# Kernel optimization log

Hardware: AMD Instinct MI355X
Metric: run time of the kernel (lower is better)

Reference implementation:

```python
import jax, jax.numpy as jnp
import numpy as np

B, R, N, D = 8, 5, 1024, 512  # batch, relations, utterances per dialogue, d_model
LN_EPS = 1e-5


def setup_inputs() -> dict:
    key = jax.random.key(0)
    k1, k2, k3 = jax.random.split(key, 3)
    h = jax.random.normal(k1, (B, N, D), dtype=jnp.float32)
    # Binary adjacency: adj[b, r, v, u] = 1 means u sends a message to v under relation r.
    adj = (jax.random.uniform(k2, (B, R, N, N)) < 0.5).astype(jnp.float32)
    # Relation 0 is the self-loop relation (identity), as in build_adjacency.
    adj = adj.at[:, 0].set(jnp.broadcast_to(jnp.eye(N, dtype=jnp.float32), (B, N, N)))
    # Per-relation Linear (bias=False) weights, torch convention: y = x @ W_r.T, W_r: (D, D)
    W = jax.random.normal(k3, (R, D, D), dtype=jnp.float32) * 0.02
    gamma = jnp.ones((D,), dtype=jnp.float32)
    beta = jnp.zeros((D,), dtype=jnp.float32)
    return {"h": h, "adj": adj, "W": W, "gamma": gamma, "beta": beta}


def reference(h, adj, W, gamma, beta):
    # Degree-normalize each relation's adjacency (row-normalized mean aggregation).
    deg = jnp.clip(jnp.sum(adj, axis=-1, keepdims=True), 1.0)  # (B,R,N,1)
    A = adj / deg
    # Mean aggregation per relation: (B,R,N,N) @ (B,N,D) -> (B,R,N,D)
    msg = jnp.einsum('brvu,bud->brvd', A, h)
    # Per-relation linear (x @ W_r.T) and sum over relations: (B,N,D)
    agg = jnp.einsum('brvd,red->bve', msg, W)
    # Dropout is identity in eval mode; ReLU, residual, LayerNorm.
    out = jax.nn.relu(agg) + h
    mu = jnp.mean(out, axis=-1, keepdims=True)
    xc = out - mu
    var = jnp.mean(xc * xc, axis=-1, keepdims=True)
    return xc / jnp.sqrt(var + LN_EPS) * gamma + beta
```

## Files before the change

kernel.cpp:

```cpp
#include <hip/hip_runtime.h>
#include <stdint.h>

#define Bd 8
#define Rr 5
#define Nn 1024
#define Dd 512
#define KK (Rr*Dd)

typedef __attribute__((ext_vector_type(8))) short bf16x8;
typedef __attribute__((ext_vector_type(4))) float f32x4;
typedef unsigned short u16;

__device__ __forceinline__ u16 f2bf(float x){
  union { float f; unsigned u; } v; v.f = x;
  unsigned r = v.u + 0x7FFFu + ((v.u >> 16) & 1u);
  return (u16)(r >> 16);
}

__device__ __forceinline__ void gll16(const void* g, void* l){
  __builtin_amdgcn_global_load_lds(
      (const __attribute__((address_space(1))) void*)g,
      (__attribute__((address_space(3))) void*)l, 16, 0, 0);
}

__global__ __launch_bounds__(256) void k_prep(
    const float* __restrict__ h, const float* __restrict__ W,
    u16* __restrict__ hTp, u16* __restrict__ Wt2, u16* __restrict__ msg){
  __shared__ float t32[32][65];
  const int tid = threadIdx.x;
  const int g = blockIdx.x;
  if (g < 2048){
    const int ut  = g & 31;
    const int dtg = (g >> 5) & 7;
    const int b   = g >> 8;
    const float* hb = h + ((size_t)b*Nn + (size_t)ut*32)*Dd + dtg*64;
    #pragma unroll
    for (int j=0;j<8;j++){
      int e = j*256 + tid;
      int ul = e >> 6, dl = e & 63;
      t32[ul][dl] = hb[(size_t)ul*Dd + dl];
    }
    __syncthreads();
    u16* ob = hTp + (size_t)b*Dd*Nn;
    #pragma unroll
    for (int j=0;j<8;j++){
      int e = j*256 + tid;
      int dtl = e >> 9;
      int rem = e & 511;
      int dr = rem >> 5, uu = rem & 31;
      int dt = dtg*4 + dtl;
      ob[((size_t)ut*32 + dt)*512 + rem] = f2bf(t32[uu][dtl*16 + dr]);
    }
  } else if (g < 3328){
    int idx = (g - 2048)*1024 + tid*4;
    int e = idx / KK;
    int k = idx % KK;
    int ri = (k < 2048) ? (1 + (k >> 9)) : 0;
    int d = k & 511;
    f32x4 w = *(const f32x4*)(W + (((size_t)ri*Dd + e)*Dd + d));
    u16 o[4] = { f2bf(w.x), f2bf(w.y), f2bf(w.z), f2bf(w.w) };
    *(uint2*)(Wt2 + idx) = *(uint2*)o;
  } else {
    int q = g - 3328;
    int row = q*4 + (tid >> 6);
    int d0 = (tid & 63)*8;
    f32x4 a = *(const f32x4*)(h + (size_t)row*Dd + d0);
    f32x4 c = *(const f32x4*)(h + (size_t)row*Dd + d0 + 4);
    bf16x8 pk;
    pk[0]=(short)f2bf(a.x); pk[1]=(short)f2bf(a.y);
    pk[2]=(short)f2bf(a.z); pk[3]=(short)f2bf(a.w);
    pk[4]=(short)f2bf(c.x); pk[5]=(short)f2bf(c.y);
    pk[6]=(short)f2bf(c.z); pk[7]=(short)f2bf(c.w);
    *(bf16x8*)(msg + (size_t)row*KK + 2048 + d0) = pk;
  }
}

__global__ __launch_bounds__(512,2) void k_msg(
    const float* __restrict__ adj, const u16* __restrict__ hTp,
    u16* __restrict__ msg){
  __shared__ __align__(16) u16 sA[2][4][32*64];
  __shared__ float sT[16*516];
  __shared__ float sDeg[4][32];

  const int tid  = threadIdx.x;
  const int lane = tid & 63;
  const int wave = tid >> 6;
  const int b  = blockIdx.x & 7;
  const int vt = blockIdx.x >> 3;
  const int v0 = vt * 32;
  const float* adjb = adj + (((size_t)b*Rr + 1)*Nn + v0)*Nn;
  const u16* hTpb = hTp + (size_t)b*Dd*Nn;

  const int srow = tid >> 4;
  const int sc   = tid & 15;
  const size_t aoff = (size_t)srow*Nn + sc*4;
  const int wslot = sc ^ ((srow & 7) << 1);

  float deg[4] = {0.f,0.f,0.f,0.f};
  f32x4 aregA[4], aregB[4];
  f32x4 acc[4][2][4];
  #pragma unroll
  for (int ri=0;ri<4;ri++)
    #pragma unroll
    for (int m=0;m<2;m++)
      #pragma unroll
      for (int n=0;n<4;n++) acc[ri][m][n] = (f32x4){0.f,0.f,0.f,0.f};

  const int rlo = lane & 15, ch = lane >> 4;
  const int boff = rlo*32 + ch*8;

  #define AISSUE(DST, T) do {                                                 \
    _Pragma("unroll")                                                         \
    for (int ri=0;ri<4;ri++)                                                  \
      DST[ri] = *(const f32x4*)(adjb + (size_t)ri*Nn*Nn + (size_t)(T)*64 + aoff); \
  } while(0)

  #define PACK(SRC, BUFI) do {                                                \
    _Pragma("unroll")                                                         \
    for (int ri=0;ri<4;ri++){                                                 \
      f32x4 p = SRC[ri];                                                      \
      deg[ri] += p.x+p.y+p.z+p.w;                                             \
      uint2 pk;                           \
      pk.x = (__float_as_uint(p.x)>>16) | (__float_as_uint(p.y) & 0xFFFF0000u);\
      pk.y = (__float_as_uint(p.z)>>16) | (__float_as_uint(p.w) & 0xFFFF0000u);\
      *(uint2*)((char*)sA[BUFI][ri] + srow*128 + wslot*8) = pk;               \
    }                                                                         \
  } while(0)

  #define LOADB(DST, T) do {                                                  \
    _Pragma("unroll")                                                         \
    for (int kk=0;kk<2;kk++){                                                 \
      const u16* bp = hTpb + ((((size_t)((T)*2+kk))*32 + (wave<<2))<<9) + boff;\
      _Pragma("unroll")                                                       \
      for (int n=0;n<4;n++)                                                   \
        DST[kk][n] = *(const bf16x8*)(bp + ((size_t)n<<9));                   \
    }                                                                         \
  } while(0)

  #define MSTEP(BFR, BUFI) do {                                               \
    const char* abase = (const char*)sA[BUFI];                                \
    _Pragma("unroll")                                                         \
    for (int kk=0;kk<2;kk++){                                                 \
      _Pragma("unroll")                                                       \
      for (int ri=0;ri<4;ri++){                                               \
        bf16x8 af[2];                                                         \
        _Pragma("unroll")                                                     \
        for (int m=0;m<2;m++){                                                \
          const int row = m*16 + rlo;                                         \
          af[m] = *(const bf16x8*)(abase + ri*4096 + row*128                  \
                    + (((kk*8 + ch*2) ^ ((row&7)<<1))<<3));                   \
        }                                                                     \
        _Pragma("unroll")                                                     \
        for (int m=0;m<2;m++)                                                 \
          _Pragma("unroll")                                                   \
          for (int n=0;n<4;n++)                                               \
            acc[ri][m][n] = __builtin_amdgcn_mfma_f32_16x16x32_bf16(          \
                af[m], BFR[kk][n], acc[ri][m][n], 0, 0, 0);                   \
      }                                                                       \
    }                                                                         \
  } while(0)

  #define STEP_BARRIER() do {                                                 \
    asm volatile("s_waitcnt lgkmcnt(0)" ::: "memory");                        \
    __builtin_amdgcn_sched_barrier(0);                                        \
    __builtin_amdgcn_s_barrier();                                             \
    __builtin_amdgcn_sched_barrier(0);                                        \
  } while(0)

  AISSUE(aregA, 0);
  PACK(aregA, 0);
  __syncthreads();
  AISSUE(aregA, 1);

  for (int t = 0; t < 14; t += 2){
    {
      bf16x8 bfr[2][4];
      LOADB(bfr, t);
      AISSUE(aregB, t+2);
      PACK(aregA, 1);
      MSTEP(bfr, 0);
      STEP_BARRIER();
    }
    {
      bf16x8 bfr[2][4];
      LOADB(bfr, t+1);
      AISSUE(aregA, t+3);
      PACK(aregB, 0);
      MSTEP(bfr, 1);
      STEP_BARRIER();
    }
  }
  {
    bf16x8 bfr[2][4];
    LOADB(bfr, 14);
    PACK(aregA, 1);
    MSTEP(bfr, 0);
    STEP_BARRIER();
  }
  {
    bf16x8 bfr[2][4];
    LOADB(bfr, 15);
    MSTEP(bfr, 1);
  }
  #undef AISSUE
  #undef PACK
  #undef LOADB
  #undef MSTEP
  #undef STEP_BARRIER

  #pragma unroll
  for (int ri=0;ri<4;ri++){
    float d = deg[ri];
    d += __shfl_xor(d, 1); d += __shfl_xor(d, 2);
    d += __shfl_xor(d, 4); d += __shfl_xor(d, 8);
    if (sc == 0) sDeg[ri][srow] = d;
  }
  __syncthreads();

  u16* mb = msg + ((size_t)b*Nn + v0)*KK;
  #pragma unroll
  for (int ri=0;ri<4;ri++){
    #pragma unroll
    for (int hh=0;hh<2;hh++){
      #pragma unroll
      for (int reg=0;reg<4;reg++){
        const int rl = ch*4 + reg;
        const float inv = 1.0f / fmaxf(sDeg[ri][hh*16 + rl], 1.0f);
        #pragma unroll
        for (int n=0;n<4;n++){
          const int col = (wave<<6) + n*16 + rlo;
          const int colw = col ^ (((col>>5)&7)<<2);
          sT[rl*516 + colw] = acc[ri][hh][n][reg] * inv;
        }
      }
      __syncthreads();
      #pragma unroll
      for (int s=0;s<2;s++){
        const int rl = wave*2 + s;
        const int m5 = lane >> 2;
        const int e  = m5 & 7;
        const int j0 = (2*lane) & 7;
        f32x4 lo = *(const f32x4*)&sT[rl*516 + (m5<<5) + (((j0  ) ^ e)<<2)];
        f32x4 hi = *(const f32x4*)&sT[rl*516 + (m5<<5) + (((j0+1) ^ e)<<2)];
        bf16x8 pk;
        pk[0]=(short)f2bf(lo.x); pk[1]=(short)f2bf(lo.y);
        pk[2]=(short)f2bf(lo.z); pk[3]=(short)f2bf(lo.w);
        pk[4]=(short)f2bf(hi.x); pk[5]=(short)f2bf(hi.y);
        pk[6]=(short)f2bf(hi.z); pk[7]=(short)f2bf(hi.w);
        *(bf16x8*)(mb + (size_t)(hh*16 + rl)*KK + ri*512 + lane*8) = pk;
      }
      __syncthreads();
    }
  }
}

__global__ __launch_bounds__(512,4) void k_agg(
    const u16* __restrict__ msg, const u16* __restrict__ Wt,
    float* __restrict__ agg){
  __shared__ __align__(16) u16 sA[2][64*64];
  __shared__ __align__(16) u16 sB[2][128*64];
  const int tid = threadIdx.x;
  const int lane = tid & 63, wave = tid >> 6;
  const int wm = wave >> 2, wn = wave & 3;
  const int g = blockIdx.x;
  const int et = g >> 7;
  const int bv = g & 127;
  const int b  = bv >> 4;
  const int vt = bv & 15;
  const int v0 = vt*64, e0 = et*128;
  const u16* Ab = msg + ((size_t)b*Nn + v0)*KK;
  const u16* Bb = Wt + (size_t)e0*KK;

  f32x4 acc[2][2];
  #pragma unroll
  for (int m=0;m<2;m++)
    #pragma unroll
    for (int n=0;n<2;n++) acc[m][n] = (f32x4){0.f,0.f,0.f,0.f};

  #define STAGE(buf, kt) do {                                              \
    { int c = tid; int row_ = c>>3, chg = (c&7) ^ (row_&7);                \
      gll16(Ab + (size_t)row_*KK + (kt)*64 + chg*8,                        \
            (char*)sA[buf] + ((size_t)(wave<<6))*16); }                    \
    _Pragma("unroll")                                                      \
    for (int i=0;i<2;i++){                                                 \
      int c = i*512 + tid; int row_ = c>>3, chg = (c&7) ^ (row_&7);        \
      gll16(Bb + (size_t)row_*KK + (kt)*64 + chg*8,                        \
            (char*)sB[buf] + ((size_t)(i*512 + (wave<<6)))*16);            \
    }                                                                      \
  } while(0)

  STAGE(0, 0);
  __syncthreads();

  const int ch = lane >> 4, rlo = lane & 15;

  for (int kt = 0; kt < KK/64; ++kt){
    if (kt < KK/64 - 1) STAGE((kt+1)&1, kt+1);
    const char* a  = (const char*)sA[kt&1];
    const char* bb = (const char*)sB[kt&1];
    #pragma unroll
    for (int kk=0; kk<2; ++kk){
      bf16x8 af[2], bfx[2];
      #pragma unroll
      for (int m=0;m<2;m++){
        const int row = wm*32 + m*16 + rlo;
        af[m] = *(const bf16x8*)(a + row*128 + ((((kk<<2)+ch) ^ (row&7))<<4));
      }
      #pragma unroll
      for (int n=0;n<2;n++){
        const int row = wn*32 + n*16 + rlo;
        bfx[n] = *(const bf16x8*)(bb + row*128 + ((((kk<<2)+ch) ^ (row&7))<<4));
      }
      #pragma unroll
      for (int m=0;m<2;m++)
        #pragma unroll
        for (int n=0;n<2;n++)
          acc[m][n] = __builtin_amdgcn_mfma_f32_16x16x32_bf16(af[m], bfx[n], acc[m][n], 0, 0, 0);
    }
    __syncthreads();
  }
  #undef STAGE

  float* ob = agg + ((size_t)b*Nn + v0)*Dd + e0;
  #pragma unroll
  for (int m=0;m<2;m++)
    #pragma unroll
    for (int reg=0;reg<4;reg++){
      const int row = wm*32 + m*16 + ((lane>>4)<<2) + reg;
      #pragma unroll
      for (int n=0;n<2;n++){
        const int col = wn*32 + n*16 + (lane & 15);
        ob[(size_t)row*Dd + col] = acc[m][n][reg];
      }
    }
}

__global__ __launch_bounds__(256,4) void k_ln(
    const float* __restrict__ agg, const float* __restrict__ h,
    const float* __restrict__ gamma, const float* __restrict__ beta,
    float* __restrict__ out){
  const int row = blockIdx.x*4 + (threadIdx.x >> 6);
  const int lane = threadIdx.x & 63;
  const float* a  = agg + (size_t)row*Dd;
  const float* hh = h   + (size_t)row*Dd;
  float x[8];
  float sum = 0.f, sq = 0.f;
  #pragma unroll
  for (int q=0;q<2;q++){
    f32x4 av = *(const f32x4*)(a  + ((size_t)q*64+lane)*4);
    f32x4 hv = *(const f32x4*)(hh + ((size_t)q*64+lane)*4);
    #pragma unroll
    for (int k=0;k<4;k++){
      float v = fmaxf(av[k], 0.f) + hv[k];
      x[q*4+k] = v; sum += v; sq += v*v;
    }
  }
  #pragma unroll
  for (int off=32; off; off>>=1){
    sum += __shfl_xor(sum, off);
    sq  += __shfl_xor(sq,  off);
  }
  const float mu  = sum * (1.f/(float)Dd);
  const float var = sq * (1.f/(float)Dd) - mu*mu;
  const float rstd = rsqrtf(var + 1e-5f);
  float* o = out + (size_t)row*Dd;
  #pragma unroll
  for (int q=0;q<2;q++){
    f32x4 g  = *(const f32x4*)(gamma + ((size_t)q*64+lane)*4);
    f32x4 be = *(const f32x4*)(beta  + ((size_t)q*64+lane)*4);
    f32x4 ov;
    #pragma unroll
    for (int k=0;k<4;k++)
      ov[k] = (x[q*4+k] - mu) * rstd * g[k] + be[k];
    *(f32x4*)(o + ((size_t)q*64+lane)*4) = ov;
  }
}

extern "C" void kernel_launch(void* const* d_in, const int* in_sizes, int n_in,
                              void* d_out, int out_size, void* d_ws, size_t ws_size,
                              hipStream_t stream){
  const float* h     = (const float*)d_in[0];
  const float* adj   = (const float*)d_in[1];
  const float* W     = (const float*)d_in[2];
  const float* gamma = (const float*)d_in[3];
  const float* beta  = (const float*)d_in[4];
  float* out = (float*)d_out;
  char* ws = (char*)d_ws;

  u16*  hTp = (u16*)(ws);
  u16*  Wt2 = (u16*)(ws + 8388608);
  u16*  msg = (u16*)(ws + 11010048);
  float* agg = (float*)(ws + 52953088);

  k_prep<<<dim3(5376), dim3(256), 0, stream>>>(h, W, hTp, Wt2, msg);
  k_msg <<<dim3(Bd*32), dim3(512), 0, stream>>>(adj, hTp, msg);
  k_agg <<<dim3(Bd*(Nn/64)*(Dd/128)), dim3(512), 0, stream>>>(msg, Wt2, agg);
  k_ln  <<<dim3(Bd*Nn/4), dim3(256), 0, stream>>>(agg, h, gamma, beta, out);
}
```

Measured before the change: 95.23 us.

## Split message kernel across D halves with 256-thread blocks and single-buffered loop

Each k_msg block now handles 32 rows and half of the feature dimension with 256 threads, doubling the grid to 512 blocks. The adjacency staging uses 8-float loads per thread with 16-byte LDS writes, the main loop is rewritten into one software-pipelined loop with priority boost around MFMAs, and the epilogue uses a simpler unswizzled transpose with 4-byte stores. This aims to raise occupancy and parallelism, but it reads every adjacency tile twice (once per D half), relying on cache to absorb the duplicate traffic.

```diff
diff --git a/kernel.cpp b/kernel.cpp
--- a/kernel.cpp
+++ b/kernel.cpp
@@ -10,6 +10,7 @@
 typedef __attribute__((ext_vector_type(8))) short bf16x8;
 typedef __attribute__((ext_vector_type(4))) float f32x4;
 typedef unsigned short u16;
+typedef unsigned int u32;
 
 __device__ __forceinline__ u16 f2bf(float x){
   union { float f; unsigned u; } v; v.f = x;
@@ -75,29 +76,32 @@
   }
 }
 
-__global__ __launch_bounds__(512,2) void k_msg(
+__global__ __launch_bounds__(256,2) void k_msg(
     const float* __restrict__ adj, const u16* __restrict__ hTp,
     u16* __restrict__ msg){
   __shared__ __align__(16) u16 sA[2][4][32*64];
-  __shared__ float sT[16*516];
+  __shared__ float sT[16*260];
   __shared__ float sDeg[4][32];
 
   const int tid  = threadIdx.x;
   const int lane = tid & 63;
   const int wave = tid >> 6;
-  const int b  = blockIdx.x & 7;
-  const int vt = blockIdx.x >> 3;
+  const int bid = blockIdx.x;
+  const int dhalf = bid >> 8;
+  const int bv = bid & 255;
+  const int b  = bv >> 5;
+  const int vt = bv & 31;
   const int v0 = vt * 32;
   const float* adjb = adj + (((size_t)b*Rr + 1)*Nn + v0)*Nn;
   const u16* hTpb = hTp + (size_t)b*Dd*Nn;
 
-  const int srow = tid >> 4;
-  const int sc   = tid & 15;
-  const size_t aoff = (size_t)srow*Nn + sc*4;
-  const int wslot = sc ^ ((srow & 7) << 1);
+  const int srow = tid >> 3;
+  const int sc   = tid & 7;
+  const size_t aoff = (size_t)srow*Nn + sc*8;
+  const int wslot = sc ^ (srow & 7);
 
   float deg[4] = {0.f,0.f,0.f,0.f};
-  f32x4 aregA[4], aregB[4];
+  f32x4 ar0[4], ar1[4];
   f32x4 acc[4][2][4];
   #pragma unroll
   for (int ri=0;ri<4;ri++)
@@ -109,36 +113,44 @@
   const int rlo = lane & 15, ch = lane >> 4;
   const int boff = rlo*32 + ch*8;
 
-  #define AISSUE(DST, T) do {                                                 \
-    _Pragma("unroll")                                                         \
-    for (int ri=0;ri<4;ri++)                                                  \
-      DST[ri] = *(const f32x4*)(adjb + (size_t)ri*Nn*Nn + (size_t)(T)*64 + aoff); \
-  } while(0)
-
-  #define PACK(SRC, BUFI) do {                                                \
+  #define AISSUE(T) do {                                                      \
     _Pragma("unroll")                                                         \
     for (int ri=0;ri<4;ri++){                                                 \
-      f32x4 p = SRC[ri];                                                      \
-      deg[ri] += p.x+p.y+p.z+p.w;                                             \
-      uint2 pk;                           \
-      pk.x = (__float_as_uint(p.x)>>16) | (__float_as_uint(p.y) & 0xFFFF0000u);\
-      pk.y = (__float_as_uint(p.z)>>16) | (__float_as_uint(p.w) & 0xFFFF0000u);\
-      *(uint2*)((char*)sA[BUFI][ri] + srow*128 + wslot*8) = pk;               \
+      const float* ap = adjb + (size_t)ri*Nn*Nn + (size_t)(T)*64 + aoff;      \
+      ar0[ri] = *(const f32x4*)ap;                                            \
+      ar1[ri] = *(const f32x4*)(ap + 4);                                      \
     }                                                                         \
   } while(0)
 
-  #define LOADB(DST, T) do {                                                  \
+  #define PACK(BUFI) do {                                                     \
+    _Pragma("unroll")                                                         \
+    for (int ri=0;ri<4;ri++){                                                 \
+      f32x4 p0 = ar0[ri], p1 = ar1[ri];                                       \
+      deg[ri] += p0.x+p0.y+p0.z+p0.w + p1.x+p1.y+p1.z+p1.w;                   \
+      uint4 pk;                           \
+      pk.x = (__float_as_uint(p0.x)>>16) | (__float_as_uint(p0.y) & 0xFFFF0000u);\
+      pk.y = (__float_as_uint(p0.z)>>16) | (__float_as_uint(p0.w) & 0xFFFF0000u);\
+      pk.z = (__float_as_uint(p1.x)>>16) | (__float_as_uint(p1.y) & 0xFFFF0000u);\
+      pk.w = (__float_as_uint(p1.z)>>16) | (__float_as_uint(p1.w) & 0xFFFF0000u);\
+      *(uint4*)((char*)sA[BUFI][ri] + srow*128 + (wslot<<4)) = pk;            \
+    }                                                                         \
+  } while(0)
+
+  #define LOADB(T) do {                                                       \
     _Pragma("unroll")                                                         \
     for (int kk=0;kk<2;kk++){                                                 \
-      const u16* bp = hTpb + ((((size_t)((T)*2+kk))*32 + (wave<<2))<<9) + boff;\
       _Pragma("unroll")                                                       \
-      for (int n=0;n<4;n++)                                                   \
-        DST[kk][n] = *(const bf16x8*)(bp + ((size_t)n<<9));                   \
+      for (int n=0;n<4;n++){                                                  \
+        const int dt = dhalf*16 + (wave<<2) + n;                              \
+        bfr[kk][n] = *(const bf16x8*)(hTpb +                                  \
+            (((size_t)((T)*2+kk)*32 + dt)<<9) + boff);                        \
+      }                                                                       \
     }                                                                         \
   } while(0)
 
-  #define MSTEP(BFR, BUFI) do {                                               \
+  #define MSTEP(BUFI) do {                                                    \
     const char* abase = (const char*)sA[BUFI];                                \
+    __builtin_amdgcn_s_setprio(1);                                            \
     _Pragma("unroll")                                                         \
     for (int kk=0;kk<2;kk++){                                                 \
       _Pragma("unroll")                                                       \
@@ -147,72 +159,61 @@
         _Pragma("unroll")                                                     \
         for (int m=0;m<2;m++){                                                \
           const int row = m*16 + rlo;                                         \
+          const int g = kk*4 + ch;                                            \
           af[m] = *(const bf16x8*)(abase + ri*4096 + row*128                  \
-                    + (((kk*8 + ch*2) ^ ((row&7)<<1))<<3));                   \
+                    + ((g ^ (row&7))<<4));                                    \
         }                                                                     \
         _Pragma("unroll")                                                     \
         for (int m=0;m<2;m++)                                                 \
           _Pragma("unroll")                                                   \
           for (int n=0;n<4;n++)                                               \
             acc[ri][m][n] = __builtin_amdgcn_mfma_f32_16x16x32_bf16(          \
-                af[m], BFR[kk][n], acc[ri][m][n], 0, 0, 0);                   \
+                af[m], bfr[kk][n], acc[ri][m][n], 0, 0, 0);                   \
       }                                                                       \
     }                                                                         \
-  } while(0)
-
+    __builtin_amdgcn_s_setprio(0);                                            \
+  } while(0)
+
+  #define FENCE() __builtin_amdgcn_sched_barrier(0)
   #define STEP_BARRIER() do {                                                 \
     asm volatile("s_waitcnt lgkmcnt(0)" ::: "memory");                        \
-    __builtin_amdgcn_sched_barrier(0);                                        \
+    FENCE();                                                                  \
     __builtin_amdgcn_s_barrier();                                             \
-    __builtin_amdgcn_sched_barrier(0);                                        \
-  } while(0)
-
-  AISSUE(aregA, 0);
-  PACK(aregA, 0);
+    FENCE();                                                                  \
+  } while(0)
+
+  bf16x8 bfr[2][4];
+
+  AISSUE(0);
+  PACK(0);
   __syncthreads();
-  AISSUE(aregA, 1);
-
-  for (int t = 0; t < 14; t += 2){
-    {
-      bf16x8 bfr[2][4];
-      LOADB(bfr, t);
-      AISSUE(aregB, t+2);
-      PACK(aregA, 1);
-      MSTEP(bfr, 0);
-      STEP_BARRIER();
-    }
-    {
-      bf16x8 bfr[2][4];
-      LOADB(bfr, t+1);
-      AISSUE(aregA, t+3);
-      PACK(aregB, 0);
-      MSTEP(bfr, 1);
-      STEP_BARRIER();
-    }
-  }
-  {
-    bf16x8 bfr[2][4];
-    LOADB(bfr, 14);
-    PACK(aregA, 1);
-    MSTEP(bfr, 0);
+  AISSUE(1);
+  FENCE();
+  LOADB(0);
+  FENCE();
+
+  for (int t = 0; t < 15; ++t){
+    PACK((t+1)&1);
+    FENCE();
+    if (t < 14) AISSUE(t+2);
+    FENCE();
+    MSTEP(t&1);
+    FENCE();
+    LOADB(t+1);
     STEP_BARRIER();
   }
-  {
-    bf16x8 bfr[2][4];
-    LOADB(bfr, 15);
-    MSTEP(bfr, 1);
-  }
+  MSTEP(1);
   #undef AISSUE
   #undef PACK
   #undef LOADB
   #undef MSTEP
+  #undef FENCE
   #undef STEP_BARRIER
 
   #pragma unroll
   for (int ri=0;ri<4;ri++){
     float d = deg[ri];
-    d += __shfl_xor(d, 1); d += __shfl_xor(d, 2);
-    d += __shfl_xor(d, 4); d += __shfl_xor(d, 8);
+    d += __shfl_xor(d, 1); d += __shfl_xor(d, 2); d += __shfl_xor(d, 4);
     if (sc == 0) sDeg[ri][srow] = d;
   }
   __syncthreads();
@@ -229,25 +230,22 @@
         #pragma unroll
         for (int n=0;n<4;n++){
           const int col = (wave<<6) + n*16 + rlo;
-          const int colw = col ^ (((col>>5)&7)<<2);
-          sT[rl*516 + colw] = acc[ri][hh][n][reg] * inv;
+          sT[rl*260 + col] = acc[ri][hh][n][reg] * inv;
         }
       }
       __syncthreads();
-      #pragma unroll
-      for (int s=0;s<2;s++){
-        const int rl = wave*2 + s;
-        const int m5 = lane >> 2;
-        const int e  = m5 & 7;
-        const int j0 = (2*lane) & 7;
-        f32x4 lo = *(const f32x4*)&sT[rl*516 + (m5<<5) + (((j0  ) ^ e)<<2)];
-        f32x4 hi = *(const f32x4*)&sT[rl*516 + (m5<<5) + (((j0+1) ^ e)<<2)];
-        bf16x8 pk;
-        pk[0]=(short)f2bf(lo.x); pk[1]=(short)f2bf(lo.y);
-        pk[2]=(short)f2bf(lo.z); pk[3]=(short)f2bf(lo.w);
-        pk[4]=(short)f2bf(hi.x); pk[5]=(short)f2bf(hi.y);
-        pk[6]=(short)f2bf(hi.z); pk[7]=(short)f2bf(hi.w);
-        *(bf16x8*)(mb + (size_t)(hh*16 + rl)*KK + ri*512 + lane*8) = pk;
+      {
+        const int row = tid >> 4;
+        const int base = tid & 15;
+        u16* orow = mb + (size_t)(hh*16 + row)*KK + ri*512 + dhalf*256;
+        #pragma unroll
+        for (int j=0;j<8;j++){
+          const int unit = base + 16*j;
+          float lo = sT[row*260 + 2*unit];
+          float hi = sT[row*260 + 2*unit + 1];
+          u32 pk = (u32)f2bf(lo) | ((u32)f2bf(hi) << 16);
+          *(u32*)(orow + 2*unit) = pk;
+        }
       }
       __syncthreads();
     }
@@ -393,7 +391,7 @@
   float* agg = (float*)(ws + 52953088);
 
   k_prep<<<dim3(5376), dim3(256), 0, stream>>>(h, W, hTp, Wt2, msg);
-  k_msg <<<dim3(Bd*32), dim3(512), 0, stream>>>(adj, hTp, msg);
+  k_msg <<<dim3(512), dim3(256), 0, stream>>>(adj, hTp, msg);
   k_agg <<<dim3(Bd*(Nn/64)*(Dd/128)), dim3(512), 0, stream>>>(msg, Wt2, agg);
   k_ln  <<<dim3(Bd*Nn/4), dim3(256), 0, stream>>>(agg, h, gamma, beta, out);
 }
```

New measurement: 107.8 us. 1.13x slower.
